# Optimization experiments

Hardware: AMD Instinct MI355X
Metric: run time of the kernel (lower is better)

The kernel has to match this reference:

```python
import jax, jax.numpy as jnp
import numpy as np

N = 256
M = 180


def _fft3_centered(u):
    # centered 3D FFT: shift so that frequency 0 is at index n//2
    return jnp.fft.fftshift(jnp.fft.fftn(jnp.fft.ifftshift(u)))


def _ifft2_centered(s):
    ax = (-2, -1)
    return jnp.fft.fftshift(jnp.fft.ifft2(jnp.fft.ifftshift(s, axes=ax), axes=ax), axes=ax)


def _trilinear(F, pos):
    """Sample complex 3D grid F (n,n,n) at fractional index positions pos (...,3).
    Points outside the grid contribute zero (frequencies beyond Nyquist)."""
    n = F.shape[0]
    p0f = jnp.floor(pos)
    f = pos - p0f                      # fractional part, in [0,1)
    p0 = p0f.astype(jnp.int32)
    acc = jnp.zeros(pos.shape[:-1], dtype=F.dtype)
    for dx in (0, 1):
        for dy in (0, 1):
            for dz in (0, 1):
                idx = p0 + jnp.array([dx, dy, dz], jnp.int32)
                w = ((f[..., 0] if dx else 1.0 - f[..., 0])
                     * (f[..., 1] if dy else 1.0 - f[..., 1])
                     * (f[..., 2] if dz else 1.0 - f[..., 2]))
                valid = jnp.all((idx >= 0) & (idx < n), axis=-1)
                idc = jnp.clip(idx, 0, n - 1)
                val = F[idc[..., 0], idc[..., 1], idc[..., 2]]  # irregular gather
                acc = acc + jnp.where(valid, w, 0.0) * val
    return acc


def _lamino_fwd(weight, theta, tilt):
    """NUFFT laminography forward projector (Fourier-slice formulation).
    weight: (n,n,n,2) real/imag volume; theta: (M,) angles; tilt: scalar.
    Returns (M,n,n,2) projections, matching tike's Lamino.fwd math: the 2D
    Fourier transform of each projection equals the 3D FT of the volume
    sampled on a plane tilted by `tilt` and rotated by `theta` about z."""
    n = weight.shape[0]
    u = jax.lax.complex(weight[..., 0], weight[..., 1])
    F = _fft3_centered(u)                                   # (n,n,n) complex64
    fr = ((jnp.arange(n) - n // 2) / n).astype(jnp.float32)  # [-0.5, 0.5)
    kv, ku = jnp.meshgrid(fr, fr, indexing='ij')            # detector freq grid
    ct, st = jnp.cos(theta), jnp.sin(theta)                 # (M,)
    cp_, sp = jnp.cos(tilt), jnp.sin(tilt)
    one = jnp.ones_like(ct)
    e_u = jnp.stack([ct, st, 0.0 * ct], -1)                 # (M,3) horizontal axis
    e_v = jnp.stack([-st * cp_, ct * cp_, sp * one], -1)    # (M,3) tilted axis
    # 3D non-uniform frequencies for every (angle, detector pixel): (M,n,n,3)
    k3 = ku[None, :, :, None] * e_u[:, None, None, :] + kv[None, :, :, None] * e_v[:, None, None, :]
    pos = k3 * n + n // 2                                   # fractional grid coords
    samples = _trilinear(F, pos)                            # (M,n,n) complex
    proj = _ifft2_centered(samples)                         # (M,n,n) complex
    return jnp.stack([proj.real, proj.imag], -1).astype(jnp.float32)


def setup_inputs() -> dict:
    key = jax.random.key(0)
    k1, k2 = jax.random.split(key)
    weight = jax.random.normal(k1, (N, N, N, 2), dtype=jnp.float32)
    theta = jax.random.uniform(k2, (M,), dtype=jnp.float32) * (2.0 * np.pi)
    tilt = jnp.float32(1.0)  # laminography tilt angle (rad); source default pi/2
    return {"weight": weight, "theta": theta, "tilt": tilt}


def reference(weight, theta, tilt):
    return _lamino_fwd(weight, theta, tilt)
```

## Files before the change

kernel.cpp:

```cpp
#include <hip/hip_runtime.h>
#include <math.h>


namespace {

template<int MODE, bool INV>
__global__ __launch_bounds__(256)
void fft_pass(const float2* in, float2* out) {
  __shared__ float sre[8][265];
  __shared__ float sim[8][265];
  __shared__ float twr[128];
  __shared__ float twi[128];
  const int t = threadIdx.x;
  if (t < 128) {
    const float TWO_PI = 6.28318530717958647692f;
    float ang = (INV ? TWO_PI : -TWO_PI) * ((float)t * (1.0f / 256.0f));
    float s, c;
    sincosf(ang, &s, &c);
    twr[t] = c;
    twi[t] = s;
  }
  int l, j0, base, stride;
  if (MODE == 0) { l = t >> 5; j0 = t & 31; }
  else           { l = t & 7;  j0 = t >> 3; }
  const int lineIdx = (int)blockIdx.x * 8 + l;
  if (MODE == 0)      { base = lineIdx * 256;                            stride = 1;     }
  else if (MODE == 1) { base = (lineIdx >> 8) * 65536 + (lineIdx & 255); stride = 256;   }
  else                { base = lineIdx;                                  stride = 65536; }

  #pragma unroll
  for (int r = 0; r < 8; r++) {
    int j = j0 + 32 * r;
    float2 v = in[base + j * stride];
    float sgn = (j & 1) ? -1.0f : 1.0f;
    sre[l][j] = v.x * sgn;
    sim[l][j] = v.y * sgn;
  }
  __syncthreads();

  const int line = t >> 5;
  const int lane = t & 31;
  #pragma unroll
  for (int s = 0; s < 8; s++) {
    const int half = 128 >> s;
    #pragma unroll
    for (int r = 0; r < 4; r++) {
      int b   = lane + 32 * r;
      int pos = b & (half - 1);
      int grp = b >> (7 - s);
      int i   = (grp << (8 - s)) + pos;
      int j   = i + half;
      float ar = sre[line][i], ai = sim[line][i];
      float br = sre[line][j], bi = sim[line][j];
      sre[line][i] = ar + br;
      sim[line][i] = ai + bi;
      float dr = ar - br, di = ai - bi;
      int mm = pos << s;
      float wr = twr[mm], wi = twi[mm];
      sre[line][j] = dr * wr - di * wi;
      sim[line][j] = dr * wi + di * wr;
    }
    __syncthreads();
  }

  const float scale = INV ? (1.0f / 256.0f) : 1.0f;
  #pragma unroll
  for (int r = 0; r < 8; r++) {
    int j = j0 + 32 * r;
    int rev = (int)(__brev((unsigned)j) >> 24);
    float sgn = (j & 1) ? -scale : scale;
    float2 v;
    v.x = sre[l][rev] * sgn;
    v.y = sim[l][rev] * sgn;
    out[base + j * stride] = v;
  }
}

__global__ __launch_bounds__(256)
void sample_kernel(const float2* __restrict__ F, float2* __restrict__ out,
                   const float* __restrict__ theta, const float* __restrict__ tiltp) {
  const int m = blockIdx.z;
  const int b = blockIdx.x * 16 + threadIdx.x;
  const int a = blockIdx.y * 16 + threadIdx.y;
  float th = theta[m];
  float ct = cosf(th), st = sinf(th);
  float tl = tiltp[0];
  float cp = cosf(tl), sp = sinf(tl);
  float bu = (float)(b - 128);
  float av = (float)(a - 128);
  float p0 = bu * ct + av * (-st * cp) + 128.0f;
  float p1 = bu * st + av * (ct * cp) + 128.0f;
  float p2 = av * sp + 128.0f;
  float f0 = floorf(p0), f1 = floorf(p1), f2 = floorf(p2);
  int x0 = (int)f0, y0 = (int)f1, z0 = (int)f2;
  float fx = p0 - f0, fy = p1 - f1, fz = p2 - f2;
  float accr = 0.0f, acci = 0.0f;
  #pragma unroll
  for (int dx = 0; dx < 2; dx++) {
    int x = x0 + dx;
    bool vx = (x >= 0) && (x < 256);
    int xc = min(max(x, 0), 255);
    float wx = dx ? fx : (1.0f - fx);
    #pragma unroll
    for (int dy = 0; dy < 2; dy++) {
      int y = y0 + dy;
      bool vy = vx && (y >= 0) && (y < 256);
      int yc = min(max(y, 0), 255);
      float wxy = wx * (dy ? fy : (1.0f - fy));
      int rowbase = (xc * 256 + yc) * 256;
      #pragma unroll
      for (int dz = 0; dz < 2; dz++) {
        int z = z0 + dz;
        bool v = vy && (z >= 0) && (z < 256);
        int zc = min(max(z, 0), 255);
        float w = v ? wxy * (dz ? fz : (1.0f - fz)) : 0.0f;
        float2 c = F[rowbase + zc];
        accr += w * c.x;
        acci += w * c.y;
      }
    }
  }
  out[(m * 256 + a) * 256 + b] = make_float2(accr, acci);
}

}

extern "C" void kernel_launch(void* const* d_in, const int* in_sizes, int n_in,
                              void* d_out, int out_size, void* d_ws, size_t ws_size,
                              hipStream_t stream) {
  const float2* w  = (const float2*)d_in[0];
  const float*  th = (const float*)d_in[1];
  const float*  tl = (const float*)d_in[2];
  float2* F    = (float2*)d_ws;
  float2* out2 = (float2*)d_out;

  fft_pass<0, false><<<8192, 256, 0, stream>>>(w, F);
  fft_pass<1, false><<<8192, 256, 0, stream>>>(F, F);
  fft_pass<2, false><<<8192, 256, 0, stream>>>(F, F);

  dim3 g(16, 16, 180), blk(16, 16);
  sample_kernel<<<g, blk, 0, stream>>>(F, out2, th, tl);

  fft_pass<0, true><<<5760, 256, 0, stream>>>(out2, out2);
  fft_pass<1, true><<<5760, 256, 0, stream>>>(out2, out2);
}
```

Baseline: 646.4 us.

## Batch 16 lines per block for strided FFT passes and vectorize sampling

The strided FFT passes (y and z axes) now process 16 lines per block instead of 8. Each row of 16 consecutive threads therefore reads 16 contiguous complex values (128 bytes) rather than 8, which improves coalescing of the large-stride memory accesses. The trilinear sampling kernel now computes 4 adjacent detector pixels per thread: it hoists the z and tilt terms out of the per-pixel work, uses sincosf, and writes results as two float4 stores. The trade-offs are more shared memory per block and fewer threads overall in the sampler, which may lower occupancy and latency hiding for the irregular gathers.

```diff
diff --git a/kernel.cpp b/kernel.cpp
--- a/kernel.cpp
+++ b/kernel.cpp
@@ -4,9 +4,9 @@
 
 namespace {
 
-template<int MODE, bool INV>
+template<bool INV>
 __global__ __launch_bounds__(256)
-void fft_pass(const float2* in, float2* out) {
+void fft_pass0(const float2* in, float2* out) {
   __shared__ float sre[8][265];
   __shared__ float sim[8][265];
   __shared__ float twr[128];
@@ -20,18 +20,15 @@
     twr[t] = c;
     twi[t] = s;
   }
-  int l, j0, base, stride;
-  if (MODE == 0) { l = t >> 5; j0 = t & 31; }
-  else           { l = t & 7;  j0 = t >> 3; }
+  const int l = t >> 5;
+  const int j0 = t & 31;
   const int lineIdx = (int)blockIdx.x * 8 + l;
-  if (MODE == 0)      { base = lineIdx * 256;                            stride = 1;     }
-  else if (MODE == 1) { base = (lineIdx >> 8) * 65536 + (lineIdx & 255); stride = 256;   }
-  else                { base = lineIdx;                                  stride = 65536; }
+  const int base = lineIdx * 256;
 
   #pragma unroll
   for (int r = 0; r < 8; r++) {
     int j = j0 + 32 * r;
-    float2 v = in[base + j * stride];
+    float2 v = in[base + j];
     float sgn = (j & 1) ? -1.0f : 1.0f;
     sre[l][j] = v.x * sgn;
     sim[l][j] = v.y * sgn;
@@ -72,6 +69,77 @@
     float2 v;
     v.x = sre[l][rev] * sgn;
     v.y = sim[l][rev] * sgn;
+    out[base + j] = v;
+  }
+}
+
+template<int MODE, bool INV>
+__global__ __launch_bounds__(256)
+void fft_pass16(const float2* in, float2* out) {
+  __shared__ float sre[16][264];
+  __shared__ float sim[16][264];
+  __shared__ float twr[128];
+  __shared__ float twi[128];
+  const int t = threadIdx.x;
+  if (t < 128) {
+    const float TWO_PI = 6.28318530717958647692f;
+    float ang = (INV ? TWO_PI : -TWO_PI) * ((float)t * (1.0f / 256.0f));
+    float s, c;
+    sincosf(ang, &s, &c);
+    twr[t] = c;
+    twi[t] = s;
+  }
+  const int l  = t & 15;
+  const int j0 = t >> 4;
+  const int lineIdx = (int)blockIdx.x * 16 + l;
+  int base, stride;
+  if (MODE == 1) { base = (lineIdx >> 8) * 65536 + (lineIdx & 255); stride = 256;   }
+  else           { base = lineIdx;                                  stride = 65536; }
+
+  #pragma unroll
+  for (int r = 0; r < 16; r++) {
+    int j = j0 + 16 * r;
+    float2 v = in[base + j * stride];
+    float sgn = (j & 1) ? -1.0f : 1.0f;
+    sre[l][j] = v.x * sgn;
+    sim[l][j] = v.y * sgn;
+  }
+  __syncthreads();
+
+  const int line = t >> 4;
+  const int lane = t & 15;
+  #pragma unroll
+  for (int s = 0; s < 8; s++) {
+    const int half = 128 >> s;
+    #pragma unroll
+    for (int r = 0; r < 8; r++) {
+      int b   = lane + 16 * r;
+      int pos = b & (half - 1);
+      int grp = b >> (7 - s);
+      int i   = (grp << (8 - s)) + pos;
+      int jj  = i + half;
+      float ar = sre[line][i], ai = sim[line][i];
+      float br = sre[line][jj], bi = sim[line][jj];
+      sre[line][i] = ar + br;
+      sim[line][i] = ai + bi;
+      float dr = ar - br, di = ai - bi;
+      int mm = pos << s;
+      float wr = twr[mm], wi = twi[mm];
+      sre[line][jj] = dr * wr - di * wi;
+      sim[line][jj] = dr * wi + di * wr;
+    }
+    __syncthreads();
+  }
+
+  const float scale = INV ? (1.0f / 256.0f) : 1.0f;
+  #pragma unroll
+  for (int r = 0; r < 16; r++) {
+    int j = j0 + 16 * r;
+    int rev = (int)(__brev((unsigned)j) >> 24);
+    float sgn = (j & 1) ? -scale : scale;
+    float2 v;
+    v.x = sre[l][rev] * sgn;
+    v.y = sim[l][rev] * sgn;
     out[base + j * stride] = v;
   }
 }
@@ -79,48 +147,69 @@
 __global__ __launch_bounds__(256)
 void sample_kernel(const float2* __restrict__ F, float2* __restrict__ out,
                    const float* __restrict__ theta, const float* __restrict__ tiltp) {
-  const int m = blockIdx.z;
-  const int b = blockIdx.x * 16 + threadIdx.x;
-  const int a = blockIdx.y * 16 + threadIdx.y;
-  float th = theta[m];
-  float ct = cosf(th), st = sinf(th);
-  float tl = tiltp[0];
-  float cp = cosf(tl), sp = sinf(tl);
-  float bu = (float)(b - 128);
-  float av = (float)(a - 128);
-  float p0 = bu * ct + av * (-st * cp) + 128.0f;
-  float p1 = bu * st + av * (ct * cp) + 128.0f;
-  float p2 = av * sp + 128.0f;
-  float f0 = floorf(p0), f1 = floorf(p1), f2 = floorf(p2);
-  int x0 = (int)f0, y0 = (int)f1, z0 = (int)f2;
-  float fx = p0 - f0, fy = p1 - f1, fz = p2 - f2;
-  float accr = 0.0f, acci = 0.0f;
-  #pragma unroll
-  for (int dx = 0; dx < 2; dx++) {
-    int x = x0 + dx;
-    bool vx = (x >= 0) && (x < 256);
-    int xc = min(max(x, 0), 255);
-    float wx = dx ? fx : (1.0f - fx);
+  const int m  = blockIdx.z;
+  const int a  = blockIdx.y * 16 + threadIdx.y;
+  const int b0 = blockIdx.x * 64 + threadIdx.x * 4;
+  const float th = theta[m];
+  float st, ct;
+  sincosf(th, &st, &ct);
+  const float tl = tiltp[0];
+  float sp, cp;
+  sincosf(tl, &sp, &cp);
+
+  const float av = (float)(a - 128);
+  const float p2 = av * sp + 128.0f;
+  const float f2 = floorf(p2);
+  const int   z0 = (int)f2;
+  const float fz = p2 - f2;
+  const int   z1 = z0 + 1;
+  const bool vz0 = (z0 >= 0) & (z0 < 256);
+  const bool vz1 = (z1 >= 0) & (z1 < 256);
+  const int  zc0 = min(max(z0, 0), 255);
+  const int  zc1 = min(max(z1, 0), 255);
+  const float p0b = av * (-st * cp) + 128.0f;
+  const float p1b = av * (ct * cp) + 128.0f;
+
+  float2 res[4];
+  #pragma unroll
+  for (int i = 0; i < 4; i++) {
+    const float bu = (float)(b0 + i - 128);
+    const float p0 = bu * ct + p0b;
+    const float p1 = bu * st + p1b;
+    const float f0 = floorf(p0), f1 = floorf(p1);
+    const int x0 = (int)f0, y0 = (int)f1;
+    const float fx = p0 - f0, fy = p1 - f1;
+    float accr = 0.0f, acci = 0.0f;
     #pragma unroll
-    for (int dy = 0; dy < 2; dy++) {
-      int y = y0 + dy;
-      bool vy = vx && (y >= 0) && (y < 256);
-      int yc = min(max(y, 0), 255);
-      float wxy = wx * (dy ? fy : (1.0f - fy));
-      int rowbase = (xc * 256 + yc) * 256;
+    for (int dx = 0; dx < 2; dx++) {
+      const int x = x0 + dx;
+      const bool vx = (x >= 0) & (x < 256);
+      const int xc = min(max(x, 0), 255);
+      const float wx = dx ? fx : (1.0f - fx);
       #pragma unroll
-      for (int dz = 0; dz < 2; dz++) {
-        int z = z0 + dz;
-        bool v = vy && (z >= 0) && (z < 256);
-        int zc = min(max(z, 0), 255);
-        float w = v ? wxy * (dz ? fz : (1.0f - fz)) : 0.0f;
-        float2 c = F[rowbase + zc];
-        accr += w * c.x;
-        acci += w * c.y;
+      for (int dy = 0; dy < 2; dy++) {
+        const int y = y0 + dy;
+        const bool vy = vx & (y >= 0) & (y < 256);
+        const int yc = min(max(y, 0), 255);
+        const float wxy = wx * (dy ? fy : (1.0f - fy));
+        const int rowbase = (xc * 256 + yc) * 256;
+        {
+          const float w0 = (vy & vz0) ? wxy * (1.0f - fz) : 0.0f;
+          const float2 c = F[rowbase + zc0];
+          accr += w0 * c.x; acci += w0 * c.y;
+        }
+        {
+          const float w1 = (vy & vz1) ? wxy * fz : 0.0f;
+          const float2 c = F[rowbase + zc1];
+          accr += w1 * c.x; acci += w1 * c.y;
+        }
       }
     }
-  }
-  out[(m * 256 + a) * 256 + b] = make_float2(accr, acci);
+    res[i] = make_float2(accr, acci);
+  }
+  float4* o = (float4*)(&out[((size_t)(m * 256 + a)) * 256 + b0]);
+  o[0] = make_float4(res[0].x, res[0].y, res[1].x, res[1].y);
+  o[1] = make_float4(res[2].x, res[2].y, res[3].x, res[3].y);
 }
 
 }
@@ -134,13 +223,13 @@
   float2* F    = (float2*)d_ws;
   float2* out2 = (float2*)d_out;
 
-  fft_pass<0, false><<<8192, 256, 0, stream>>>(w, F);
-  fft_pass<1, false><<<8192, 256, 0, stream>>>(F, F);
-  fft_pass<2, false><<<8192, 256, 0, stream>>>(F, F);
-
-  dim3 g(16, 16, 180), blk(16, 16);
+  fft_pass0<false><<<8192, 256, 0, stream>>>(w, F);
+  fft_pass16<1, false><<<4096, 256, 0, stream>>>(F, F);
+  fft_pass16<2, false><<<4096, 256, 0, stream>>>(F, F);
+
+  dim3 g(4, 16, 180), blk(16, 16);
   sample_kernel<<<g, blk, 0, stream>>>(F, out2, th, tl);
 
-  fft_pass<0, true><<<5760, 256, 0, stream>>>(out2, out2);
-  fft_pass<1, true><<<5760, 256, 0, stream>>>(out2, out2);
-}
+  fft_pass0<true><<<5760, 256, 0, stream>>>(out2, out2);
+  fft_pass16<1, true><<<2880, 256, 0, stream>>>(out2, out2);
+}
```

After: 809.2 us. +25.2%, slower.
